# Kernel tuning notes

Measured on AMD Instinct MI355X. Metric: run time of the kernel, lower is better.

## Reference

```python
import jax, jax.numpy as jnp
import numpy as np

NUM_HEADS = 16


def setup_inputs() -> dict:
    key = jax.random.key(0)
    k = jax.random.split(key, 5)
    b, s, h = 2, 2048, 1024
    scale = 1.0 / np.sqrt(h)
    return {
        "x": jax.random.normal(k[0], (b, s, h), dtype=jnp.float32),
        "W_qkv": jax.random.normal(k[1], (h, 3 * h), dtype=jnp.float32) * scale,
        "b_qkv": jax.random.normal(k[2], (3 * h,), dtype=jnp.float32) * 0.02,
        "W_o": jax.random.normal(k[3], (h, h), dtype=jnp.float32) * scale,
        "b_o": jax.random.normal(k[4], (h,), dtype=jnp.float32) * 0.02,
    }


def _mha_causal(Q, K, V, num_heads):
    b, s, hd = Q.shape
    d_head = hd // num_heads
    # b s (n h) -> b n s h
    _Q = Q.reshape(b, s, num_heads, d_head).transpose(0, 2, 1, 3)
    _K = K.reshape(b, s, num_heads, d_head).transpose(0, 2, 1, 3)
    _V = V.reshape(b, s, num_heads, d_head).transpose(0, 2, 1, 3)
    scores = jnp.einsum('bnqh,bnkh->bnqk', _Q, _K)
    causal = jnp.tril(jnp.ones((s, s), dtype=bool))  # True where allowed
    scores = jnp.where(causal, scores, -jnp.inf) / jnp.sqrt(jnp.float32(d_head))
    A = jax.nn.softmax(scores, axis=-1)
    AV = jnp.einsum('bnqk,bnkh->bnqh', A, _V)
    return AV.transpose(0, 2, 1, 3).reshape(b, s, hd)


def reference(x, W_qkv, b_qkv, W_o, b_o):
    qkv = x @ W_qkv + b_qkv  # [b, s, 3h]
    Q, K, V = jnp.split(qkv, 3, axis=-1)
    attn = _mha_causal(Q, K, V, NUM_HEADS)
    return attn @ W_o + b_o
```

## Files before the change

### kernel.cpp

```cpp
#include <hip/hip_runtime.h>
#include <hip/hip_bf16.h>

typedef unsigned short u16;
typedef __attribute__((ext_vector_type(8))) short short8;
typedef __attribute__((ext_vector_type(4))) float f32x4;
typedef __attribute__((ext_vector_type(16))) float f32x16;
typedef __attribute__((ext_vector_type(4))) float float4v;
typedef __attribute__((ext_vector_type(4))) unsigned int uint4v;
typedef __attribute__((ext_vector_type(2))) unsigned int uint2v;

__device__ __forceinline__ u16 f2bf(float f) {
    union { float f; unsigned u; } x;
    x.f = f;
    unsigned r = x.u + 0x7fffu + ((x.u >> 16) & 1u);
    return (u16)(r >> 16);
}

__device__ __forceinline__ unsigned cvtpk(float lo, float hi) {
    unsigned r;
    asm("v_cvt_pk_bf16_f32 %0, %1, %2" : "=v"(r) : "v"(lo), "v"(hi));
    return r;
}

__device__ __forceinline__ void gload16(const u16* g, u16* l) {
    __builtin_amdgcn_global_load_lds(
        (const __attribute__((address_space(1))) unsigned*)g,
        (__attribute__((address_space(3))) unsigned*)l, 16, 0, 0);
}

#define WAITV(n) asm volatile("s_waitcnt vmcnt(" #n ")" ::: "memory")

__global__ __launch_bounds__(256) void cast_f32_bf16(
    const float* __restrict__ src, u16* __restrict__ dst, int n8) {
    int i = blockIdx.x * 256 + threadIdx.x;
    if (i >= n8) return;
    const float4v* s = (const float4v*)(src + (size_t)i * 8);
    float4v a = s[0], b = s[1];
    uint4v o;
    o[0] = (unsigned)f2bf(a[0]) | ((unsigned)f2bf(a[1]) << 16);
    o[1] = (unsigned)f2bf(a[2]) | ((unsigned)f2bf(a[3]) << 16);
    o[2] = (unsigned)f2bf(b[0]) | ((unsigned)f2bf(b[1]) << 16);
    o[3] = (unsigned)f2bf(b[2]) | ((unsigned)f2bf(b[3]) << 16);
    *(uint4v*)(dst + (size_t)i * 8) = o;
}

__global__ __launch_bounds__(256) void transpose_f32_bf16(
    const float* __restrict__ src, u16* __restrict__ dst, int R, int C) {
    __shared__ __align__(16) u16 tile[64][72];
    int tr = blockIdx.x * 64;
    int tc = blockIdx.y * 64;
    int t = threadIdx.x;
    int r = t >> 2;
    int c4 = (t & 3) * 16;
    const float4v* sp = (const float4v*)(src + (size_t)(tr + r) * C + tc + c4);
#pragma unroll
    for (int v = 0; v < 4; v++) {
        float4v x = sp[v];
#pragma unroll
        for (int j = 0; j < 4; j++) tile[r][c4 + v * 4 + j] = f2bf(x[j]);
    }
    __syncthreads();
    u16* dp = dst + (size_t)(tc + r) * R + tr + c4;
#pragma unroll
    for (int i = 0; i < 16; i++) dp[i] = tile[c4 + i][r];
}

__global__ __launch_bounds__(256) void build_kv(
    const u16* __restrict__ qkv, u16* __restrict__ kv) {
    int bh = blockIdx.y;
    int tt = blockIdx.x;
    int b = bh >> 4, h = bh & 15;
    u16* outb = kv + (size_t)bh * 262144 + (size_t)tt * 8192;
    __shared__ __align__(16) u16 tile[64][72];
    int t = threadIdx.x;
    int r = t >> 2;
    int c4 = (t & 3) * 16;
    const u16* srow = qkv + (size_t)(b * 2048 + tt * 64 + r) * 3072 + h * 64;
    *(uint4v*)&outb[r * 64 + c4]     = *(const uint4v*)(srow + 1024 + c4);
    *(uint4v*)&outb[r * 64 + c4 + 8] = *(const uint4v*)(srow + 1024 + c4 + 8);
    *(uint4v*)&tile[r][c4]     = *(const uint4v*)(srow + 2048 + c4);
    *(uint4v*)&tile[r][c4 + 8] = *(const uint4v*)(srow + 2048 + c4 + 8);
    __syncthreads();
    u16* dp = outb + 4096 + r * 64 + c4;
#pragma unroll
    for (int i = 0; i < 16; i++) dp[i] = tile[c4 + i][r];
}

template <int BN, bool OUT_BF16>
__global__ __launch_bounds__(256) void gemm_kernel(
    const u16* __restrict__ A, const u16* __restrict__ BT,
    const float* __restrict__ bias, void* __restrict__ Cout,
    int M, int N, int K) {
    constexpr int NF = BN / 32;
    __shared__ __align__(16) u16 As[3][128 * 32];
    __shared__ __align__(16) u16 Bs[3][BN * 32];
    int bm = blockIdx.x, bn = blockIdx.y;
    int t = threadIdx.x;
    int lane = t & 63, wave = t >> 6;
    int wr = wave >> 1, wc = wave & 1;
    f32x4 acc[4][NF] = {};

    const u16* gA = A + (size_t)(bm * 128) * K;
    const u16* gB = BT + (size_t)(bn * BN) * K;

    auto stage = [&](int buf, int k0) {
#pragma unroll
        for (int i = 0; i < 2; i++) {
            int o = i * 4096 + t * 16;
            int row = o >> 6;
            int cb = (o & 63) ^ (((row >> 1) & 3) << 4);
            gload16(gA + (size_t)row * K + k0 + (cb >> 1),
                    &As[buf][i * 2048 + (t & 192) * 8]);
        }
#pragma unroll
        for (int i = 0; i < BN / 64; i++) {
            int o = i * 4096 + t * 16;
            int row = o >> 6;
            int cb = (o & 63) ^ (((row >> 1) & 3) << 4);
            gload16(gB + (size_t)row * K + k0 + (cb >> 1),
                    &Bs[buf][i * 2048 + (t & 192) * 8]);
        }
    };

    stage(0, 0);
    stage(1, 32);
    if constexpr (BN == 128) WAITV(4); else WAITV(3);
    __builtin_amdgcn_sched_barrier(0);
    __builtin_amdgcn_s_barrier();
    __builtin_amdgcn_sched_barrier(0);

    int nk = K >> 5;
    for (int tt = 0; tt < nk; tt++) {
        bool pre = (tt + 2 < nk);
        if (pre) stage((tt + 2) % 3, (tt + 2) << 5);
        int row16 = lane & 15;
        int colb = ((lane >> 4) * 16) ^ (((row16 >> 1) & 3) << 4);
        const u16* Ab = As[tt % 3];
        const u16* Bb = Bs[tt % 3];
        short8 af[4], bf[NF];
#pragma unroll
        for (int m = 0; m < 4; m++)
            af[m] = *(const short8*)&Ab[(wr * 64 + m * 16 + row16) * 32 + (colb >> 1)];
#pragma unroll
        for (int n = 0; n < NF; n++)
            bf[n] = *(const short8*)&Bb[(wc * (BN / 2) + n * 16 + row16) * 32 + (colb >> 1)];
        __builtin_amdgcn_s_setprio(1);
#pragma unroll
        for (int m = 0; m < 4; m++)
#pragma unroll
            for (int n = 0; n < NF; n++)
                acc[m][n] = __builtin_amdgcn_mfma_f32_16x16x32_bf16(
                    af[m], bf[n], acc[m][n], 0, 0, 0);
        __builtin_amdgcn_s_setprio(0);
        if (pre) { if constexpr (BN == 128) WAITV(4); else WAITV(3); }
        else     { WAITV(0); }
        __builtin_amdgcn_sched_barrier(0);
        __builtin_amdgcn_s_barrier();
        __builtin_amdgcn_sched_barrier(0);
    }

#pragma unroll
    for (int m = 0; m < 4; m++) {
#pragma unroll
        for (int n = 0; n < NF; n++) {
            int col = bn * BN + wc * (BN / 2) + n * 16 + (lane & 15);
            float bv = bias ? bias[col] : 0.f;
#pragma unroll
            for (int r = 0; r < 4; r++) {
                int row = bm * 128 + wr * 64 + m * 16 + (lane >> 4) * 4 + r;
                float v = acc[m][n][r] + bv;
                if constexpr (OUT_BF16)
                    ((u16*)Cout)[(size_t)row * N + col] = f2bf(v);
                else
                    ((float*)Cout)[(size_t)row * N + col] = v;
            }
        }
    }
}

__global__ __launch_bounds__(256, 2) void attn_kernel(
    const u16* __restrict__ qkv, const u16* __restrict__ kv,
    u16* __restrict__ attn, float* __restrict__ part_o,
    float* __restrict__ part_l) {
    int bid = blockIdx.x;
    int bh = bid & 31;
    int j = 23 - (bid >> 5);
    int sp, tbeg, tend, kc = 0;
    bool partial;
    if (j >= 8) {
        int idx = j - 8;
        sp = 8 + (idx >> 1);
        kc = idx & 1;
        int half = sp + 1;
        partial = true;
        tbeg = kc ? half : 0;
        tend = kc ? 2 * sp + 2 : half;
    } else {
        sp = j;
        partial = false;
        tbeg = 0;
        tend = 2 * sp + 2;
    }
    int b = bh >> 4, h = bh & 15;
    int t = threadIdx.x;
    int lane = t & 63, w = t >> 6;
    int qb = sp * 128 + w * 32;
    int kend = qb + 32;
    int l31 = lane & 31, hi32 = lane >> 5;
    int swz = (lane & 7) << 4;

    __shared__ __align__(16) u16 KVb[24576];

    const u16* kvb = kv + (size_t)bh * 262144;

    auto stage = [&](int buf, int tt) {
        const char* g0 = (const char*)(kvb + (size_t)tt * 8192);
#pragma unroll
        for (int kv2 = 0; kv2 < 2; kv2++)
#pragma unroll
            for (int i = 0; i < 2; i++) {
                int o = i * 4096 + t * 16;
                int row = o >> 7;
                int cb = (o & 127) ^ ((row & 7) << 4);
                gload16((const u16*)(g0 + kv2 * 8192 + row * 128 + cb),
                        &KVb[buf * 8192 + kv2 * 4096 + i * 2048 + (t & 192) * 8]);
            }
    };

    short8 qf[4];
    {
        const u16* q0 = qkv + (size_t)(b * 2048 + qb + l31) * 3072 + h * 64 + hi32 * 8;
#pragma unroll
        for (int dd = 0; dd < 4; dd++) qf[dd] = *(const short8*)(q0 + dd * 16);
    }
    stage(tbeg % 3, tbeg);
    stage((tbeg + 1) % 3, tbeg + 1);

    float l_lane = 0.f;
    f32x16 oT[2] = {};

    const float C1 = 0.1803368880f;
    const float C2 = -17.3123404907f;

    WAITV(4);
    __builtin_amdgcn_sched_barrier(0);
    __builtin_amdgcn_s_barrier();
    __builtin_amdgcn_sched_barrier(0);

    for (int tt = tbeg; tt < tend; tt++) {
        bool pre = (tt + 2 < tend);
        if (pre) stage((tt + 2) % 3, tt + 2);
        int k0 = tt * 64;
        if (k0 < kend) {
            const u16* Ks = &KVb[(tt % 3) * 8192];
            const u16* Vs = Ks + 4096;
            f32x16 sc[2];
            __builtin_amdgcn_s_setprio(1);
#pragma unroll
            for (int kb = 0; kb < 2; kb++) {
                f32x16 z = {};
#pragma unroll
                for (int dd = 0; dd < 4; dd++) {
                    int off = (kb * 32 + l31) * 64 + (((dd * 32 + hi32 * 16) ^ swz) >> 1);
                    short8 kf = *(const short8*)&Ks[off];
                    z = __builtin_amdgcn_mfma_f32_32x32x16_bf16(kf, qf[dd], z, 0, 0, 0);
                }
                sc[kb] = z;
            }
            __builtin_amdgcn_s_setprio(0);

            float p[2][16];
            int q_g = qb + l31;
            if (k0 + 64 > qb) {
#pragma unroll
                for (int kb = 0; kb < 2; kb++)
#pragma unroll
                    for (int r = 0; r < 16; r++) {
                        int kg = k0 + kb * 32 + (r & 3) + 8 * (r >> 2) + 4 * hi32;
                        float v = (kg <= q_g) ? sc[kb][r] : -1e30f;
                        float pe = __builtin_amdgcn_exp2f(fmaf(v, C1, C2));
                        p[kb][r] = pe;
                        l_lane += pe;
                    }
            } else {
#pragma unroll
                for (int kb = 0; kb < 2; kb++)
#pragma unroll
                    for (int r = 0; r < 16; r++) {
                        float pe = __builtin_amdgcn_exp2f(fmaf(sc[kb][r], C1, C2));
                        p[kb][r] = pe;
                        l_lane += pe;
                    }
            }

            short8 pb[4];
#pragma unroll
            for (int kb = 0; kb < 2; kb++)
#pragma unroll
                for (int cset = 0; cset < 2; cset++) {
                    const float* pp = &p[kb][cset * 8];
                    unsigned A0 = cvtpk(pp[0], pp[1]);
                    unsigned A1 = cvtpk(pp[2], pp[3]);
                    unsigned A2 = cvtpk(pp[4], pp[5]);
                    unsigned A3 = cvtpk(pp[6], pp[7]);
                    unsigned za = hi32 ? A0 : A2;
                    unsigned zb = hi32 ? A1 : A3;
                    unsigned sa = (unsigned)__shfl_xor((int)za, 32, 64);
                    unsigned sb = (unsigned)__shfl_xor((int)zb, 32, 64);
                    uint4v wv;
                    wv[0] = hi32 ? sa : A0;
                    wv[1] = hi32 ? sb : A1;
                    wv[2] = hi32 ? A2 : sa;
                    wv[3] = hi32 ? A3 : sb;
                    pb[kb * 2 + cset] = __builtin_bit_cast(short8, wv);
                }

            __builtin_amdgcn_s_setprio(1);
#pragma unroll
            for (int mb = 0; mb < 2; mb++)
#pragma unroll
                for (int kk = 0; kk < 4; kk++) {
                    int off = (mb * 32 + l31) * 64 + (((kk * 32 + hi32 * 16) ^ swz) >> 1);
                    short8 vf = *(const short8*)&Vs[off];
                    oT[mb] = __builtin_amdgcn_mfma_f32_32x32x16_bf16(vf, pb[kk], oT[mb], 0, 0, 0);
                }
            __builtin_amdgcn_s_setprio(0);
        }
        if (pre) { WAITV(4); } else { WAITV(0); }
        __builtin_amdgcn_sched_barrier(0);
        __builtin_amdgcn_s_barrier();
        __builtin_amdgcn_sched_barrier(0);
    }

    if (partial) {
        int blk = (bh * 8 + (sp - 8)) * 2 + kc;
        float* po = part_o + (size_t)blk * 8192;
        int lr = w * 32 + l31;
        float lf = l_lane + __shfl_xor(l_lane, 32, 64);
        if (hi32 == 0) part_l[blk * 128 + lr] = lf;
#pragma unroll
        for (int mb = 0; mb < 2; mb++)
#pragma unroll
            for (int r = 0; r < 16; r++) {
                int d = mb * 32 + (r & 3) + 8 * (r >> 2) + 4 * hi32;
                po[lr * 64 + d] = oT[mb][r];
            }
        return;
    }

    float lf = l_lane + __shfl_xor(l_lane, 32, 64);
    float linv = __builtin_amdgcn_rcpf(lf);
    u16* ob = &KVb[w * 2304];
#pragma unroll
    for (int mb = 0; mb < 2; mb++)
#pragma unroll
        for (int rr = 0; rr < 4; rr++) {
            unsigned w0 = cvtpk(oT[mb][4 * rr] * linv, oT[mb][4 * rr + 1] * linv);
            unsigned w1 = cvtpk(oT[mb][4 * rr + 2] * linv, oT[mb][4 * rr + 3] * linv);
            int d0 = mb * 32 + rr * 8 + 4 * hi32;
            *(uint2v*)&ob[l31 * 72 + d0] = (uint2v){w0, w1};
        }
    {
        const u16* rp = &ob[l31 * 72 + hi32 * 32];
        u16* gp = attn + (size_t)(b * 2048 + qb + l31) * 1024 + h * 64 + hi32 * 32;
#pragma unroll
        for (int i = 0; i < 4; i++)
            *(uint4v*)(gp + i * 8) = *(const uint4v*)(rp + i * 8);
    }
}

__global__ __launch_bounds__(256) void attn_merge(
    const float* __restrict__ part_o, const float* __restrict__ part_l,
    u16* __restrict__ attn) {
    int bid = blockIdx.x;
    int bh = bid & 31;
    int sp8 = bid >> 5;
    int sp = sp8 + 8;
    int b = bh >> 4, h = bh & 15;
    int t = threadIdx.x;
    int blk0 = (bh * 8 + sp8) * 2;
    const float* o0 = part_o + (size_t)blk0 * 8192;
    const float* o1 = o0 + 8192;
    const float* l0 = part_l + blk0 * 128;
    const float* l1 = l0 + 128;
#pragma unroll
    for (int i = 0; i < 4; i++) {
        int r = (t >> 3) + i * 32;
        int d0 = (t & 7) * 8;
        float linv = __builtin_amdgcn_rcpf(l0[r] + l1[r]);
        const float* a = o0 + r * 64 + d0;
        const float* c = o1 + r * 64 + d0;
        uint4v w;
#pragma unroll
        for (int k = 0; k < 4; k++)
            w[k] = cvtpk((a[2 * k] + c[2 * k]) * linv,
                         (a[2 * k + 1] + c[2 * k + 1]) * linv);
        u16* gp = attn + (size_t)(b * 2048 + sp * 128 + r) * 1024 + h * 64 + d0;
        *(uint4v*)gp = w;
    }
}

extern "C" void kernel_launch(void* const* d_in, const int* in_sizes, int n_in,
                              void* d_out, int out_size, void* d_ws, size_t ws_size,
                              hipStream_t stream) {
    const float* x    = (const float*)d_in[0];
    const float* Wqkv = (const float*)d_in[1];
    const float* bqkv = (const float*)d_in[2];
    const float* Wo   = (const float*)d_in[3];
    const float* bo   = (const float*)d_in[4];
    float* out = (float*)d_out;

    char* ws = (char*)d_ws;
    u16* x_bf   = (u16*)(ws);
    u16* attnb  = (u16*)(ws);
    u16* wqkvT  = (u16*)(ws + (8ull << 20));
    u16* woT    = (u16*)(ws + (14ull << 20));
    u16* qkv    = (u16*)(ws + (16ull << 20));
    u16* kvp    = (u16*)(ws + (40ull << 20));
    float* part_o = (float*)(ws + (58ull << 20));
    float* part_l = (float*)(ws + (74ull << 20));

    cast_f32_bf16<<<2048, 256, 0, stream>>>(x, x_bf, 4096 * 1024 / 8);
    transpose_f32_bf16<<<dim3(16, 48), 256, 0, stream>>>(Wqkv, wqkvT, 1024, 3072);
    transpose_f32_bf16<<<dim3(16, 16), 256, 0, stream>>>(Wo, woT, 1024, 1024);
    gemm_kernel<128, true><<<dim3(32, 24), 256, 0, stream>>>(
        x_bf, wqkvT, bqkv, (void*)qkv, 4096, 3072, 1024);
    build_kv<<<dim3(32, 32), 256, 0, stream>>>(qkv, kvp);
    attn_kernel<<<768, 256, 0, stream>>>(qkv, kvp, attnb, part_o, part_l);
    attn_merge<<<256, 256, 0, stream>>>(part_o, part_l, attnb);
    gemm_kernel<64, false><<<dim3(32, 16), 256, 0, stream>>>(
        attnb, woT, bo, (void*)out, 4096, 1024, 1024);
}
```

Baseline: 121.5 us.

## Fuse prep kernels, write K/V layout from QKV GEMM, rebalance attention splits

Merges the cast and two transposes into a single prep launch. The QKV GEMM epilogue now writes Q and the tiled K/transposed-V layout directly, which removes the build_kv pass and the full qkv buffer. The causal attention work split changes to 1 to 4 chunks per query block to balance load, with a matching generalized merge. Attention now stages only K in shared memory and reads V fragments straight from global into registers, with occupancy hinted at 3 blocks per CU. The output is stored directly without an LDS bounce, and the risks are uncoalesced scattered epilogue stores and higher V read latency.

```diff
diff --git a/kernel.cpp b/kernel.cpp
--- a/kernel.cpp
+++ b/kernel.cpp
@@ -30,78 +30,185 @@
 
 #define WAITV(n) asm volatile("s_waitcnt vmcnt(" #n ")" ::: "memory")
 
-__global__ __launch_bounds__(256) void cast_f32_bf16(
-    const float* __restrict__ src, u16* __restrict__ dst, int n8) {
-    int i = blockIdx.x * 256 + threadIdx.x;
-    if (i >= n8) return;
-    const float4v* s = (const float4v*)(src + (size_t)i * 8);
-    float4v a = s[0], b = s[1];
-    uint4v o;
-    o[0] = (unsigned)f2bf(a[0]) | ((unsigned)f2bf(a[1]) << 16);
-    o[1] = (unsigned)f2bf(a[2]) | ((unsigned)f2bf(a[3]) << 16);
-    o[2] = (unsigned)f2bf(b[0]) | ((unsigned)f2bf(b[1]) << 16);
-    o[3] = (unsigned)f2bf(b[2]) | ((unsigned)f2bf(b[3]) << 16);
-    *(uint4v*)(dst + (size_t)i * 8) = o;
-}
-
-__global__ __launch_bounds__(256) void transpose_f32_bf16(
-    const float* __restrict__ src, u16* __restrict__ dst, int R, int C) {
+__global__ __launch_bounds__(256) void prep(
+    const float* __restrict__ x, const float* __restrict__ Wqkv,
+    const float* __restrict__ Wo, u16* __restrict__ x_bf,
+    u16* __restrict__ wqkvT, u16* __restrict__ woT) {
+    int bid = blockIdx.x;
+    int t = threadIdx.x;
+    if (bid < 2048) {
+        int i = bid * 256 + t;
+        const float4v* s = (const float4v*)(x + (size_t)i * 8);
+        float4v a = s[0], b = s[1];
+        uint4v o;
+        o[0] = (unsigned)f2bf(a[0]) | ((unsigned)f2bf(a[1]) << 16);
+        o[1] = (unsigned)f2bf(a[2]) | ((unsigned)f2bf(a[3]) << 16);
+        o[2] = (unsigned)f2bf(b[0]) | ((unsigned)f2bf(b[1]) << 16);
+        o[3] = (unsigned)f2bf(b[2]) | ((unsigned)f2bf(b[3]) << 16);
+        *(uint4v*)(x_bf + (size_t)i * 8) = o;
+        return;
+    }
+    const float* src;
+    u16* dst;
+    int C, tid;
+    if (bid < 2816) { tid = bid - 2048; src = Wqkv; dst = wqkvT; C = 3072; }
+    else            { tid = bid - 2816; src = Wo;   dst = woT;   C = 1024; }
+    int tr = (tid & 15) * 64;
+    int tc = (tid >> 4) * 64;
     __shared__ __align__(16) u16 tile[64][72];
-    int tr = blockIdx.x * 64;
-    int tc = blockIdx.y * 64;
-    int t = threadIdx.x;
     int r = t >> 2;
     int c4 = (t & 3) * 16;
     const float4v* sp = (const float4v*)(src + (size_t)(tr + r) * C + tc + c4);
 #pragma unroll
     for (int v = 0; v < 4; v++) {
-        float4v x = sp[v];
-#pragma unroll
-        for (int j = 0; j < 4; j++) tile[r][c4 + v * 4 + j] = f2bf(x[j]);
+        float4v xv = sp[v];
+#pragma unroll
+        for (int j = 0; j < 4; j++) tile[r][c4 + v * 4 + j] = f2bf(xv[j]);
     }
     __syncthreads();
-    u16* dp = dst + (size_t)(tc + r) * R + tr + c4;
+    u16* dp = dst + (size_t)(tc + r) * 1024 + tr + c4;
 #pragma unroll
     for (int i = 0; i < 16; i++) dp[i] = tile[c4 + i][r];
 }
 
-__global__ __launch_bounds__(256) void build_kv(
-    const u16* __restrict__ qkv, u16* __restrict__ kv) {
-    int bh = blockIdx.y;
-    int tt = blockIdx.x;
-    int b = bh >> 4, h = bh & 15;
-    u16* outb = kv + (size_t)bh * 262144 + (size_t)tt * 8192;
-    __shared__ __align__(16) u16 tile[64][72];
-    int t = threadIdx.x;
-    int r = t >> 2;
-    int c4 = (t & 3) * 16;
-    const u16* srow = qkv + (size_t)(b * 2048 + tt * 64 + r) * 3072 + h * 64;
-    *(uint4v*)&outb[r * 64 + c4]     = *(const uint4v*)(srow + 1024 + c4);
-    *(uint4v*)&outb[r * 64 + c4 + 8] = *(const uint4v*)(srow + 1024 + c4 + 8);
-    *(uint4v*)&tile[r][c4]     = *(const uint4v*)(srow + 2048 + c4);
-    *(uint4v*)&tile[r][c4 + 8] = *(const uint4v*)(srow + 2048 + c4 + 8);
-    __syncthreads();
-    u16* dp = outb + 4096 + r * 64 + c4;
-#pragma unroll
-    for (int i = 0; i < 16; i++) dp[i] = tile[c4 + i][r];
-}
-
-template <int BN, bool OUT_BF16>
-__global__ __launch_bounds__(256) void gemm_kernel(
+__global__ __launch_bounds__(256) void gemm_qkv(
     const u16* __restrict__ A, const u16* __restrict__ BT,
-    const float* __restrict__ bias, void* __restrict__ Cout,
-    int M, int N, int K) {
-    constexpr int NF = BN / 32;
-    __shared__ __align__(16) u16 As[3][128 * 32];
-    __shared__ __align__(16) u16 Bs[3][BN * 32];
+    const float* __restrict__ bias, u16* __restrict__ qbuf,
+    u16* __restrict__ kvp) {
+    const int K = 1024;
+    __shared__ __align__(16) u16 SMEM[24576];
     int bm = blockIdx.x, bn = blockIdx.y;
     int t = threadIdx.x;
     int lane = t & 63, wave = t >> 6;
     int wr = wave >> 1, wc = wave & 1;
-    f32x4 acc[4][NF] = {};
+    f32x4 acc[4][4] = {};
 
     const u16* gA = A + (size_t)(bm * 128) * K;
-    const u16* gB = BT + (size_t)(bn * BN) * K;
+    const u16* gB = BT + (size_t)(bn * 128) * K;
+
+    auto stage = [&](int buf, int k0) {
+#pragma unroll
+        for (int i = 0; i < 2; i++) {
+            int o = i * 4096 + t * 16;
+            int row = o >> 6;
+            int cb = (o & 63) ^ (((row >> 1) & 3) << 4);
+            gload16(gA + (size_t)row * K + k0 + (cb >> 1),
+                    &SMEM[buf * 4096 + i * 2048 + (t & 192) * 8]);
+        }
+#pragma unroll
+        for (int i = 0; i < 2; i++) {
+            int o = i * 4096 + t * 16;
+            int row = o >> 6;
+            int cb = (o & 63) ^ (((row >> 1) & 3) << 4);
+            gload16(gB + (size_t)row * K + k0 + (cb >> 1),
+                    &SMEM[12288 + buf * 4096 + i * 2048 + (t & 192) * 8]);
+        }
+    };
+
+    stage(0, 0);
+    stage(1, 32);
+    WAITV(4);
+    __builtin_amdgcn_sched_barrier(0);
+    __builtin_amdgcn_s_barrier();
+    __builtin_amdgcn_sched_barrier(0);
+
+    for (int tt = 0; tt < 32; tt++) {
+        bool pre = (tt + 2 < 32);
+        if (pre) stage((tt + 2) % 3, (tt + 2) << 5);
+        int row16 = lane & 15;
+        int colb = ((lane >> 4) * 16) ^ (((row16 >> 1) & 3) << 4);
+        const u16* Ab = &SMEM[(tt % 3) * 4096];
+        const u16* Bb = &SMEM[12288 + (tt % 3) * 4096];
+        short8 af[4], bf[4];
+#pragma unroll
+        for (int m = 0; m < 4; m++)
+            af[m] = *(const short8*)&Ab[(wr * 64 + m * 16 + row16) * 32 + (colb >> 1)];
+#pragma unroll
+        for (int n = 0; n < 4; n++)
+            bf[n] = *(const short8*)&Bb[(wc * 64 + n * 16 + row16) * 32 + (colb >> 1)];
+        __builtin_amdgcn_s_setprio(1);
+#pragma unroll
+        for (int m = 0; m < 4; m++)
+#pragma unroll
+            for (int n = 0; n < 4; n++)
+                acc[m][n] = __builtin_amdgcn_mfma_f32_16x16x32_bf16(
+                    af[m], bf[n], acc[m][n], 0, 0, 0);
+        __builtin_amdgcn_s_setprio(0);
+        if (pre) { WAITV(4); } else { WAITV(0); }
+        __builtin_amdgcn_sched_barrier(0);
+        __builtin_amdgcn_s_barrier();
+        __builtin_amdgcn_sched_barrier(0);
+    }
+
+    int l15 = lane & 15, hi = lane >> 4;
+    if (bn < 8) {
+#pragma unroll
+        for (int m = 0; m < 4; m++)
+#pragma unroll
+            for (int n = 0; n < 4; n++) {
+                int col = bn * 128 + wc * 64 + n * 16 + l15;
+                float bv = bias[col];
+#pragma unroll
+                for (int r = 0; r < 4; r++) {
+                    int row = bm * 128 + wr * 64 + m * 16 + hi * 4 + r;
+                    qbuf[(size_t)row * 1024 + col] = f2bf(acc[m][n][r] + bv);
+                }
+            }
+    } else if (bn < 16) {
+        int h2 = (bn - 8) * 2 + wc;
+#pragma unroll
+        for (int m = 0; m < 4; m++)
+#pragma unroll
+            for (int n = 0; n < 4; n++) {
+                int d = n * 16 + l15;
+                float bv = bias[1024 + h2 * 64 + d];
+#pragma unroll
+                for (int r = 0; r < 4; r++) {
+                    int row = bm * 128 + wr * 64 + m * 16 + hi * 4 + r;
+                    int b = row >> 11;
+                    int tt = (row & 2047) >> 6;
+                    int k = row & 63;
+                    kvp[(size_t)(b * 16 + h2) * 262144 + tt * 8192 + k * 64 + d] =
+                        f2bf(acc[m][n][r] + bv);
+                }
+            }
+    } else {
+        int h2 = (bn - 16) * 2 + wc;
+        int rowbase = bm * 128 + wr * 64;
+        int b = rowbase >> 11;
+        int tt = (rowbase & 2047) >> 6;
+        u16* wl = &SMEM[wave * 4608];
+#pragma unroll
+        for (int m = 0; m < 4; m++)
+#pragma unroll
+            for (int n = 0; n < 4; n++) {
+                int d = n * 16 + l15;
+                float bv = bias[2048 + h2 * 64 + d];
+                unsigned p0 = cvtpk(acc[m][n][0] + bv, acc[m][n][1] + bv);
+                unsigned p1 = cvtpk(acc[m][n][2] + bv, acc[m][n][3] + bv);
+                *(uint2v*)&wl[d * 72 + m * 16 + hi * 4] = (uint2v){p0, p1};
+            }
+        u16* dst = kvp + (size_t)(b * 16 + h2) * 262144 + tt * 8192 + 4096;
+#pragma unroll
+        for (int i = 0; i < 8; i++)
+            *(uint4v*)(dst + lane * 64 + i * 8) = *(const uint4v*)&wl[lane * 72 + i * 8];
+    }
+}
+
+__global__ __launch_bounds__(256) void gemm_out(
+    const u16* __restrict__ A, const u16* __restrict__ BT,
+    const float* __restrict__ bias, float* __restrict__ Cout) {
+    const int K = 1024, N = 1024;
+    __shared__ __align__(16) u16 As[3][4096];
+    __shared__ __align__(16) u16 Bs[3][2048];
+    int bm = blockIdx.x, bn = blockIdx.y;
+    int t = threadIdx.x;
+    int lane = t & 63, wave = t >> 6;
+    int wr = wave >> 1, wc = wave & 1;
+    f32x4 acc[4][2] = {};
+
+    const u16* gA = A + (size_t)(bm * 128) * K;
+    const u16* gB = BT + (size_t)(bn * 64) * K;
 
     auto stage = [&](int buf, int k0) {
 #pragma unroll
@@ -112,95 +219,77 @@
             gload16(gA + (size_t)row * K + k0 + (cb >> 1),
                     &As[buf][i * 2048 + (t & 192) * 8]);
         }
-#pragma unroll
-        for (int i = 0; i < BN / 64; i++) {
-            int o = i * 4096 + t * 16;
+        {
+            int o = t * 16;
             int row = o >> 6;
             int cb = (o & 63) ^ (((row >> 1) & 3) << 4);
             gload16(gB + (size_t)row * K + k0 + (cb >> 1),
-                    &Bs[buf][i * 2048 + (t & 192) * 8]);
+                    &Bs[buf][(t & 192) * 8]);
         }
     };
 
     stage(0, 0);
     stage(1, 32);
-    if constexpr (BN == 128) WAITV(4); else WAITV(3);
+    WAITV(3);
     __builtin_amdgcn_sched_barrier(0);
     __builtin_amdgcn_s_barrier();
     __builtin_amdgcn_sched_barrier(0);
 
-    int nk = K >> 5;
-    for (int tt = 0; tt < nk; tt++) {
-        bool pre = (tt + 2 < nk);
+    for (int tt = 0; tt < 32; tt++) {
+        bool pre = (tt + 2 < 32);
         if (pre) stage((tt + 2) % 3, (tt + 2) << 5);
         int row16 = lane & 15;
         int colb = ((lane >> 4) * 16) ^ (((row16 >> 1) & 3) << 4);
-        const u16* Ab = As[tt % 3];
-        const u16* Bb = Bs[tt % 3];
-        short8 af[4], bf[NF];
-#pragma unroll
-        for (int m = 0; m < 4; m++)
-            af[m] = *(const short8*)&Ab[(wr * 64 + m * 16 + row16) * 32 + (colb >> 1)];
-#pragma unroll
-        for (int n = 0; n < NF; n++)
-            bf[n] = *(const short8*)&Bb[(wc * (BN / 2) + n * 16 + row16) * 32 + (colb >> 1)];
+        short8 af[4], bf[2];
+#pragma unroll
+        for (int m = 0; m < 4; m++)
+            af[m] = *(const short8*)&As[tt % 3][(wr * 64 + m * 16 + row16) * 32 + (colb >> 1)];
+#pragma unroll
+        for (int n = 0; n < 2; n++)
+            bf[n] = *(const short8*)&Bs[tt % 3][(wc * 32 + n * 16 + row16) * 32 + (colb >> 1)];
         __builtin_amdgcn_s_setprio(1);
 #pragma unroll
         for (int m = 0; m < 4; m++)
 #pragma unroll
-            for (int n = 0; n < NF; n++)
+            for (int n = 0; n < 2; n++)
                 acc[m][n] = __builtin_amdgcn_mfma_f32_16x16x32_bf16(
                     af[m], bf[n], acc[m][n], 0, 0, 0);
         __builtin_amdgcn_s_setprio(0);
-        if (pre) { if constexpr (BN == 128) WAITV(4); else WAITV(3); }
-        else     { WAITV(0); }
+        if (pre) { WAITV(3); } else { WAITV(0); }
         __builtin_amdgcn_sched_barrier(0);
         __builtin_amdgcn_s_barrier();
         __builtin_amdgcn_sched_barrier(0);
     }
 
 #pragma unroll
-    for (int m = 0; m < 4; m++) {
-#pragma unroll
-        for (int n = 0; n < NF; n++) {
-            int col = bn * BN + wc * (BN / 2) + n * 16 + (lane & 15);
-            float bv = bias ? bias[col] : 0.f;
+    for (int m = 0; m < 4; m++)
+#pragma unroll
+        for (int n = 0; n < 2; n++) {
+            int col = bn * 64 + wc * 32 + n * 16 + (lane & 15);
+            float bv = bias[col];
 #pragma unroll
             for (int r = 0; r < 4; r++) {
                 int row = bm * 128 + wr * 64 + m * 16 + (lane >> 4) * 4 + r;
-                float v = acc[m][n][r] + bv;
-                if constexpr (OUT_BF16)
-                    ((u16*)Cout)[(size_t)row * N + col] = f2bf(v);
-                else
-                    ((float*)Cout)[(size_t)row * N + col] = v;
-            }
-        }
-    }
-}
-
-__global__ __launch_bounds__(256, 2) void attn_kernel(
-    const u16* __restrict__ qkv, const u16* __restrict__ kv,
+                Cout[(size_t)row * N + col] = acc[m][n][r] + bv;
+            }
+        }
+}
+
+__global__ __launch_bounds__(256, 3) void attn_kernel(
+    const u16* __restrict__ qbuf, const u16* __restrict__ kvp,
     u16* __restrict__ attn, float* __restrict__ part_o,
     float* __restrict__ part_l) {
     int bid = blockIdx.x;
     int bh = bid & 31;
-    int j = 23 - (bid >> 5);
-    int sp, tbeg, tend, kc = 0;
-    bool partial;
-    if (j >= 8) {
-        int idx = j - 8;
-        sp = 8 + (idx >> 1);
-        kc = idx & 1;
-        int half = sp + 1;
-        partial = true;
-        tbeg = kc ? half : 0;
-        tend = kc ? 2 * sp + 2 : half;
-    } else {
-        sp = j;
-        partial = false;
-        tbeg = 0;
-        tend = 2 * sp + 2;
-    }
+    int j = bid >> 5;
+    int sp, c, nc;
+    if (j < 4)       { sp = j;                c = 0;            nc = 1; }
+    else if (j < 12) { int i = j - 4;  sp = 4 + (i >> 1); c = i & 1; nc = 2; }
+    else if (j < 24) { int i = j - 12; sp = 8 + i / 3;    c = i % 3; nc = 3; }
+    else             { int i = j - 24; sp = 12 + (i >> 2); c = i & 3; nc = 4; }
+    int nt = 2 * sp + 2;
+    int tbeg = c * nt / nc, tend = (c + 1) * nt / nc;
+
     int b = bh >> 4, h = bh & 15;
     int t = threadIdx.x;
     int lane = t & 63, w = t >> 6;
@@ -209,32 +298,30 @@
     int l31 = lane & 31, hi32 = lane >> 5;
     int swz = (lane & 7) << 4;
 
-    __shared__ __align__(16) u16 KVb[24576];
-
-    const u16* kvb = kv + (size_t)bh * 262144;
-
-    auto stage = [&](int buf, int tt) {
+    __shared__ __align__(16) u16 Ks[3][4096];
+
+    const u16* kvb = kvp + (size_t)bh * 262144;
+
+    auto stageK = [&](int buf, int tt) {
         const char* g0 = (const char*)(kvb + (size_t)tt * 8192);
 #pragma unroll
-        for (int kv2 = 0; kv2 < 2; kv2++)
-#pragma unroll
-            for (int i = 0; i < 2; i++) {
-                int o = i * 4096 + t * 16;
-                int row = o >> 7;
-                int cb = (o & 127) ^ ((row & 7) << 4);
-                gload16((const u16*)(g0 + kv2 * 8192 + row * 128 + cb),
-                        &KVb[buf * 8192 + kv2 * 4096 + i * 2048 + (t & 192) * 8]);
-            }
+        for (int i = 0; i < 2; i++) {
+            int o = i * 4096 + t * 16;
+            int row = o >> 7;
+            int cb = (o & 127) ^ ((row & 7) << 4);
+            gload16((const u16*)(g0 + row * 128 + cb),
+                    &Ks[buf][i * 2048 + (t & 192) * 8]);
+        }
     };
 
     short8 qf[4];
     {
-        const u16* q0 = qkv + (size_t)(b * 2048 + qb + l31) * 3072 + h * 64 + hi32 * 8;
+        const u16* q0 = qbuf + (size_t)(b * 2048 + qb + l31) * 1024 + h * 64 + hi32 * 8;
 #pragma unroll
         for (int dd = 0; dd < 4; dd++) qf[dd] = *(const short8*)(q0 + dd * 16);
     }
-    stage(tbeg % 3, tbeg);
-    stage((tbeg + 1) % 3, tbeg + 1);
+    stageK(tbeg % 3, tbeg);
+    stageK((tbeg + 1) % 3, tbeg + 1);
 
     float l_lane = 0.f;
     f32x16 oT[2] = {};
@@ -242,18 +329,27 @@
     const float C1 = 0.1803368880f;
     const float C2 = -17.3123404907f;
 
-    WAITV(4);
+    WAITV(2);
     __builtin_amdgcn_sched_barrier(0);
     __builtin_amdgcn_s_barrier();
     __builtin_amdgcn_sched_barrier(0);
 
     for (int tt = tbeg; tt < tend; tt++) {
         bool pre = (tt + 2 < tend);
-        if (pre) stage((tt + 2) % 3, tt + 2);
         int k0 = tt * 64;
-        if (k0 < kend) {
-            const u16* Ks = &KVb[(tt % 3) * 8192];
-            const u16* Vs = Ks + 4096;
+        bool active = (k0 < kend);
+        short8 vf[2][4];
+        if (active) {
+            const u16* vp = kvb + (size_t)tt * 8192 + 4096;
+#pragma unroll
+            for (int mb = 0; mb < 2; mb++)
+#pragma unroll
+                for (int kk = 0; kk < 4; kk++)
+                    vf[mb][kk] = *(const short8*)(vp + (mb * 32 + l31) * 64 + kk * 16 + hi32 * 8);
+        }
+        if (pre) stageK((tt + 2) % 3, tt + 2);
+        if (active) {
+            const u16* Ksb = Ks[tt % 3];
             f32x16 sc[2];
             __builtin_amdgcn_s_setprio(1);
 #pragma unroll
@@ -262,14 +358,13 @@
 #pragma unroll
                 for (int dd = 0; dd < 4; dd++) {
                     int off = (kb * 32 + l31) * 64 + (((dd * 32 + hi32 * 16) ^ swz) >> 1);
-                    short8 kf = *(const short8*)&Ks[off];
+                    short8 kf = *(const short8*)&Ksb[off];
                     z = __builtin_amdgcn_mfma_f32_32x32x16_bf16(kf, qf[dd], z, 0, 0, 0);
                 }
                 sc[kb] = z;
             }
             __builtin_amdgcn_s_setprio(0);
 
-            float p[2][16];
             int q_g = qb + l31;
             if (k0 + 64 > qb) {
 #pragma unroll
@@ -279,7 +374,7 @@
                         int kg = k0 + kb * 32 + (r & 3) + 8 * (r >> 2) + 4 * hi32;
                         float v = (kg <= q_g) ? sc[kb][r] : -1e30f;
                         float pe = __builtin_amdgcn_exp2f(fmaf(v, C1, C2));
-                        p[kb][r] = pe;
+                        sc[kb][r] = pe;
                         l_lane += pe;
                     }
             } else {
@@ -288,21 +383,21 @@
 #pragma unroll
                     for (int r = 0; r < 16; r++) {
                         float pe = __builtin_amdgcn_exp2f(fmaf(sc[kb][r], C1, C2));
-                        p[kb][r] = pe;
+                        sc[kb][r] = pe;
                         l_lane += pe;
                     }
             }
 
-            short8 pb[4];
+            __builtin_amdgcn_s_setprio(1);
 #pragma unroll
             for (int kb = 0; kb < 2; kb++)
 #pragma unroll
                 for (int cset = 0; cset < 2; cset++) {
-                    const float* pp = &p[kb][cset * 8];
-                    unsigned A0 = cvtpk(pp[0], pp[1]);
-                    unsigned A1 = cvtpk(pp[2], pp[3]);
-                    unsigned A2 = cvtpk(pp[4], pp[5]);
-                    unsigned A3 = cvtpk(pp[6], pp[7]);
+                    int kk = kb * 2 + cset;
+                    unsigned A0 = cvtpk(sc[kb][cset * 8 + 0], sc[kb][cset * 8 + 1]);
+                    unsigned A1 = cvtpk(sc[kb][cset * 8 + 2], sc[kb][cset * 8 + 3]);
+                    unsigned A2 = cvtpk(sc[kb][cset * 8 + 4], sc[kb][cset * 8 + 5]);
+                    unsigned A3 = cvtpk(sc[kb][cset * 8 + 6], sc[kb][cset * 8 + 7]);
                     unsigned za = hi32 ? A0 : A2;
                     unsigned zb = hi32 ? A1 : A3;
                     unsigned sa = (unsigned)__shfl_xor((int)za, 32, 64);
@@ -312,61 +407,51 @@
                     wv[1] = hi32 ? sb : A1;
                     wv[2] = hi32 ? A2 : sa;
                     wv[3] = hi32 ? A3 : sb;
-                    pb[kb * 2 + cset] = __builtin_bit_cast(short8, wv);
-                }
-
-            __builtin_amdgcn_s_setprio(1);
-#pragma unroll
-            for (int mb = 0; mb < 2; mb++)
-#pragma unroll
-                for (int kk = 0; kk < 4; kk++) {
-                    int off = (mb * 32 + l31) * 64 + (((kk * 32 + hi32 * 16) ^ swz) >> 1);
-                    short8 vf = *(const short8*)&Vs[off];
-                    oT[mb] = __builtin_amdgcn_mfma_f32_32x32x16_bf16(vf, pb[kk], oT[mb], 0, 0, 0);
+                    short8 pb = __builtin_bit_cast(short8, wv);
+                    oT[0] = __builtin_amdgcn_mfma_f32_32x32x16_bf16(vf[0][kk], pb, oT[0], 0, 0, 0);
+                    oT[1] = __builtin_amdgcn_mfma_f32_32x32x16_bf16(vf[1][kk], pb, oT[1], 0, 0, 0);
                 }
             __builtin_amdgcn_s_setprio(0);
         }
-        if (pre) { WAITV(4); } else { WAITV(0); }
+        if (pre) { WAITV(2); } else { WAITV(0); }
         __builtin_amdgcn_sched_barrier(0);
         __builtin_amdgcn_s_barrier();
         __builtin_amdgcn_sched_barrier(0);
     }
 
-    if (partial) {
-        int blk = (bh * 8 + (sp - 8)) * 2 + kc;
-        float* po = part_o + (size_t)blk * 8192;
-        int lr = w * 32 + l31;
+    if (nc > 1) {
+        int off = (sp < 8) ? (sp - 4) * 2 + c
+                 : (sp < 12) ? 8 + (sp - 8) * 3 + c
+                             : 20 + (sp - 12) * 4 + c;
+        int slot = bh * 36 + off;
+        float* po = part_o + (size_t)slot * 8192;
+        int ql = w * 32 + l31;
         float lf = l_lane + __shfl_xor(l_lane, 32, 64);
-        if (hi32 == 0) part_l[blk * 128 + lr] = lf;
+        if (hi32 == 0) part_l[slot * 128 + ql] = lf;
 #pragma unroll
         for (int mb = 0; mb < 2; mb++)
 #pragma unroll
-            for (int r = 0; r < 16; r++) {
-                int d = mb * 32 + (r & 3) + 8 * (r >> 2) + 4 * hi32;
-                po[lr * 64 + d] = oT[mb][r];
+            for (int g = 0; g < 4; g++) {
+                int d0 = mb * 32 + g * 8 + hi32 * 4;
+                f32x4 v = {oT[mb][4 * g], oT[mb][4 * g + 1],
+                           oT[mb][4 * g + 2], oT[mb][4 * g + 3]};
+                *(f32x4*)(po + ql * 64 + d0) = v;
             }
         return;
     }
 
     float lf = l_lane + __shfl_xor(l_lane, 32, 64);
     float linv = __builtin_amdgcn_rcpf(lf);
-    u16* ob = &KVb[w * 2304];
+    u16* gp = attn + (size_t)(b * 2048 + qb + l31) * 1024 + h * 64;
 #pragma unroll
     for (int mb = 0; mb < 2; mb++)
 #pragma unroll
-        for (int rr = 0; rr < 4; rr++) {
-            unsigned w0 = cvtpk(oT[mb][4 * rr] * linv, oT[mb][4 * rr + 1] * linv);
-            unsigned w1 = cvtpk(oT[mb][4 * rr + 2] * linv, oT[mb][4 * rr + 3] * linv);
-            int d0 = mb * 32 + rr * 8 + 4 * hi32;
-            *(uint2v*)&ob[l31 * 72 + d0] = (uint2v){w0, w1};
-        }
-    {
-        const u16* rp = &ob[l31 * 72 + hi32 * 32];
-        u16* gp = attn + (size_t)(b * 2048 + qb + l31) * 1024 + h * 64 + hi32 * 32;
-#pragma unroll
-        for (int i = 0; i < 4; i++)
-            *(uint4v*)(gp + i * 8) = *(const uint4v*)(rp + i * 8);
-    }
+        for (int g = 0; g < 4; g++) {
+            unsigned w0 = cvtpk(oT[mb][4 * g] * linv, oT[mb][4 * g + 1] * linv);
+            unsigned w1 = cvtpk(oT[mb][4 * g + 2] * linv, oT[mb][4 * g + 3] * linv);
+            int d0 = mb * 32 + g * 8 + hi32 * 4;
+            *(uint2v*)(gp + d0) = (uint2v){w0, w1};
+        }
 }
 
 __global__ __launch_bounds__(256) void attn_merge(
@@ -374,29 +459,34 @@
     u16* __restrict__ attn) {
     int bid = blockIdx.x;
     int bh = bid & 31;
-    int sp8 = bid >> 5;
-    int sp = sp8 + 8;
+    int spi = bid >> 5;
+    int sp = spi + 4;
+    int nc = (spi < 4) ? 2 : (spi < 8) ? 3 : 4;
+    int off = (spi < 4) ? spi * 2 : (spi < 8) ? 8 + (spi - 4) * 3
+                                              : 20 + (spi - 8) * 4;
+    int slot0 = bh * 36 + off;
     int b = bh >> 4, h = bh & 15;
     int t = threadIdx.x;
-    int blk0 = (bh * 8 + sp8) * 2;
-    const float* o0 = part_o + (size_t)blk0 * 8192;
-    const float* o1 = o0 + 8192;
-    const float* l0 = part_l + blk0 * 128;
-    const float* l1 = l0 + 128;
-#pragma unroll
-    for (int i = 0; i < 4; i++) {
-        int r = (t >> 3) + i * 32;
-        int d0 = (t & 7) * 8;
-        float linv = __builtin_amdgcn_rcpf(l0[r] + l1[r]);
-        const float* a = o0 + r * 64 + d0;
-        const float* c = o1 + r * 64 + d0;
-        uint4v w;
-#pragma unroll
-        for (int k = 0; k < 4; k++)
-            w[k] = cvtpk((a[2 * k] + c[2 * k]) * linv,
-                         (a[2 * k + 1] + c[2 * k + 1]) * linv);
-        u16* gp = attn + (size_t)(b * 2048 + sp * 128 + r) * 1024 + h * 64 + d0;
-        *(uint4v*)gp = w;
+    int r = t >> 1;
+    int d0 = (t & 1) * 32;
+    float l = 0.f;
+    for (int i = 0; i < nc; i++) l += part_l[(slot0 + i) * 128 + r];
+    float linv = __builtin_amdgcn_rcpf(l);
+#pragma unroll
+    for (int g = 0; g < 4; g++) {
+        float4v s0 = {0.f, 0.f, 0.f, 0.f}, s1 = {0.f, 0.f, 0.f, 0.f};
+        for (int i = 0; i < nc; i++) {
+            const float* p = part_o + (size_t)(slot0 + i) * 8192 + r * 64 + d0 + g * 8;
+            s0 += *(const float4v*)p;
+            s1 += *(const float4v*)(p + 4);
+        }
+        uint4v wv;
+        wv[0] = cvtpk(s0[0] * linv, s0[1] * linv);
+        wv[1] = cvtpk(s0[2] * linv, s0[3] * linv);
+        wv[2] = cvtpk(s1[0] * linv, s1[1] * linv);
+        wv[3] = cvtpk(s1[2] * linv, s1[3] * linv);
+        u16* gp = attn + (size_t)(b * 2048 + sp * 128 + r) * 1024 + h * 64 + d0 + g * 8;
+        *(uint4v*)gp = wv;
     }
 }
 
@@ -415,19 +505,14 @@
     u16* attnb  = (u16*)(ws);
     u16* wqkvT  = (u16*)(ws + (8ull << 20));
     u16* woT    = (u16*)(ws + (14ull << 20));
-    u16* qkv    = (u16*)(ws + (16ull << 20));
-    u16* kvp    = (u16*)(ws + (40ull << 20));
-    float* part_o = (float*)(ws + (58ull << 20));
-    float* part_l = (float*)(ws + (74ull << 20));
-
-    cast_f32_bf16<<<2048, 256, 0, stream>>>(x, x_bf, 4096 * 1024 / 8);
-    transpose_f32_bf16<<<dim3(16, 48), 256, 0, stream>>>(Wqkv, wqkvT, 1024, 3072);
-    transpose_f32_bf16<<<dim3(16, 16), 256, 0, stream>>>(Wo, woT, 1024, 1024);
-    gemm_kernel<128, true><<<dim3(32, 24), 256, 0, stream>>>(
-        x_bf, wqkvT, bqkv, (void*)qkv, 4096, 3072, 1024);
-    build_kv<<<dim3(32, 32), 256, 0, stream>>>(qkv, kvp);
-    attn_kernel<<<768, 256, 0, stream>>>(qkv, kvp, attnb, part_o, part_l);
-    attn_merge<<<256, 256, 0, stream>>>(part_o, part_l, attnb);
-    gemm_kernel<64, false><<<dim3(32, 16), 256, 0, stream>>>(
-        attnb, woT, bo, (void*)out, 4096, 1024, 1024);
-}
+    u16* qbuf   = (u16*)(ws + (16ull << 20));
+    u16* kvp    = (u16*)(ws + (24ull << 20));
+    float* part_o = (float*)(ws + (40ull << 20));
+    float* part_l = (float*)(ws + (76ull << 20));
+
+    prep<<<3072, 256, 0, stream>>>(x, Wqkv, Wo, x_bf, wqkvT, woT);
+    gemm_qkv<<<dim3(32, 24), 256, 0, stream>>>(x_bf, wqkvT, bqkv, qbuf, kvp);
+    attn_kernel<<<1280, 256, 0, stream>>>(qbuf, kvp, attnb, part_o, part_l);
+    attn_merge<<<384, 256, 0, stream>>>(part_o, part_l, attnb);
+    gemm_out<<<dim3(32, 16), 256, 0, stream>>>(attnb, woT, bo, out);
+}
```

After: 137.0 us. 12.7% more time.
